# Kernel optimization log

Measured on AMD Instinct MI355X. Metric: run time of the kernel, lower is better.

## Reference

```python
import jax, jax.numpy as jnp
import numpy as np

LL = 1 << 20            # Fastfood padded size (power of 2 >= DD)
DD = 1024 * 768         # out_features * in_features
OUT, IN = 1024, 768


def fwht(v):
    """Unnormalized fast Walsh-Hadamard transform over a length-2^k vector."""
    n = v.shape[0]
    h = 1
    while h < n:
        v = v.reshape(-1, 2, h)
        v = jnp.concatenate([v[:, 0] + v[:, 1], v[:, 0] - v[:, 1]], axis=-1)
        h *= 2
    return v.reshape(n)


def setup_inputs() -> dict:
    key = jax.random.key(0)
    ks = jax.random.split(key, 7)
    x = jax.random.normal(ks[0], (8, 2048, IN), dtype=jnp.float32)
    theta = jax.random.normal(ks[1], (2048,), dtype=jnp.float32)
    W_0 = jax.random.normal(ks[2], (OUT, IN), dtype=jnp.float32) * 0.02
    b = jax.random.normal(ks[3], (OUT,), dtype=jnp.float32) * 0.02
    # Rademacher +/-1 diagonal
    BB = (jax.random.bernoulli(ks[4], 0.5, (LL,)).astype(jnp.float32) * 2.0 - 1.0)
    GG = jax.random.normal(ks[5], (LL,), dtype=jnp.float32)
    Pi = jax.random.permutation(ks[6], LL).astype(jnp.int64)
    return {"x": x, "theta": theta, "W_0": W_0, "b": b, "BB": BB, "GG": GG, "Pi": Pi}


def reference(x, theta, W_0, b, BB, GG, Pi):
    # pad intrinsic parameter to LL (theta.numel() < LL branch)
    theta_pad = jnp.zeros((LL,), dtype=theta.dtype).at[: theta.shape[0]].set(theta)
    # Fastfood: H B theta -> permute -> G diag -> H
    v = fwht(BB * theta_pad)
    v = v[Pi] * GG
    v = fwht(v)
    divisor = jnp.sqrt(LL * jnp.sum(GG * GG))
    update_vec = v[:DD] / (divisor * np.sqrt(float(DD) / LL))
    W_eff = W_0 + update_vec.reshape(OUT, IN)
    return jnp.einsum("bsi,oi->bso", x, W_eff) + b
```

## Files before the change

### kernel.cpp

```cpp
#include <hip/hip_runtime.h>
#include <hip/hip_bf16.h>


#define LL (1 << 20)
#define DD (1024 * 768)
#define OUTF 1024
#define INF 768
#define MROWS 16384

typedef __attribute__((ext_vector_type(8))) short s16x8;
typedef __attribute__((ext_vector_type(4))) float f32x4;
typedef __attribute__((ext_vector_type(16))) float f32x16;

__device__ __forceinline__ unsigned short f2bf(float f) {
    union { float f; unsigned u; } v; v.f = f;
    unsigned r = v.u + 0x7FFF + ((v.u >> 16) & 1);
    return (unsigned short)(r >> 16);
}

__global__ void k3_gather_fwht_lo(const int* __restrict__ Pi, const float* __restrict__ GG,
                                  const float* __restrict__ BB, const float* __restrict__ theta,
                                  const float* __restrict__ X, ushort* __restrict__ XB,
                                  float* __restrict__ T, float* __restrict__ partial) {
    __shared__ float s[1024];
    __shared__ float r01s[2048];
    __shared__ float ws4[4];
    const int tid = threadIdx.x;
    const int row = blockIdx.x;
    const int4   pv = ((const int4*)Pi)[row * 256 + tid];
    const float4 gv = ((const float4*)GG)[row * 256 + tid];
    for (int j = tid; j < 2048; j += 256) r01s[j] = BB[j] * theta[j];
    for (int h = 1; h < 1024; h <<= 1) {
        __syncthreads();
        for (int w = tid; w < 1024; w += 256) {
            int rr = w >> 9;
            int b  = w & 511;
            int bh = b & (h - 1);
            int i  = ((b - bh) << 1) + bh + rr * 1024;
            float a = r01s[i], c = r01s[i + h];
            r01s[i] = a + c; r01s[i + h] = a - c;
        }
    }
    float g2 = gv.x * gv.x + gv.y * gv.y + gv.z * gv.z + gv.w * gv.w;
    #pragma unroll
    for (int o = 32; o > 0; o >>= 1) g2 += __shfl_down(g2, o, 64);
    if ((tid & 63) == 0) ws4[tid >> 6] = g2;
    __syncthreads();
    {
        int p; float g, v;
        p = pv.x; g = gv.x;
        v = (r01s[p & 1023] + (((p >> 10) & 1) ? -1.0f : 1.0f) * r01s[1024 + (p & 1023)]) * g;
        s[tid * 4 + 0] = v;
        p = pv.y; g = gv.y;
        v = (r01s[p & 1023] + (((p >> 10) & 1) ? -1.0f : 1.0f) * r01s[1024 + (p & 1023)]) * g;
        s[tid * 4 + 1] = v;
        p = pv.z; g = gv.z;
        v = (r01s[p & 1023] + (((p >> 10) & 1) ? -1.0f : 1.0f) * r01s[1024 + (p & 1023)]) * g;
        s[tid * 4 + 2] = v;
        p = pv.w; g = gv.w;
        v = (r01s[p & 1023] + (((p >> 10) & 1) ? -1.0f : 1.0f) * r01s[1024 + (p & 1023)]) * g;
        s[tid * 4 + 3] = v;
    }
    for (int h = 1; h < 1024; h <<= 1) {
        __syncthreads();
        for (int w = tid; w < 512; w += 256) {
            int bh = w & (h - 1);
            int i  = ((w - bh) << 1) + bh;
            float a = s[i], c = s[i + h];
            s[i] = a + c; s[i + h] = a - c;
        }
    }
    __syncthreads();
    float4 v;
    v.x = s[tid * 4 + 0]; v.y = s[tid * 4 + 1]; v.z = s[tid * 4 + 2]; v.w = s[tid * 4 + 3];
    ((float4*)T)[row * 256 + tid] = v;
    if (tid == 0) partial[row] = ws4[0] + ws4[1] + ws4[2] + ws4[3];

    const float4* X4 = (const float4*)X + (size_t)row * 3072;
    ushort4* XB4 = (ushort4*)XB + (size_t)row * 3072;
    #pragma unroll
    for (int j = 0; j < 12; j++) {
        float4 xv = X4[j * 256 + tid];
        ushort4 o;
        o.x = f2bf(xv.x); o.y = f2bf(xv.y); o.z = f2bf(xv.z); o.w = f2bf(xv.w);
        XB4[j * 256 + tid] = o;
    }
}

__global__ void k4_fwht_hi(const float* __restrict__ T, const float* __restrict__ partial,
                           const float* __restrict__ W0, ushort* __restrict__ WB) {
    __shared__ float s[8 * 1025];
    __shared__ float rw[5];
    const int tid = threadIdx.x;
    float p = partial[tid] + partial[tid + 256] + partial[tid + 512] + partial[tid + 768];
    #pragma unroll
    for (int o = 32; o > 0; o >>= 1) p += __shfl_down(p, o, 64);
    if ((tid & 63) == 0) rw[tid >> 6] = p;

    const int lo0 = blockIdx.x * 8;
    const float4* T4 = (const float4*)T;
    const int hio = tid >> 1;
    const int q   = tid & 1;
    for (int hb = 0; hb < 8; hb++) {
        int hi = hb * 128 + hio;
        float4 v = T4[hi * 256 + (lo0 >> 2) + q];
        s[(4 * q + 0) * 1025 + hi] = v.x;
        s[(4 * q + 1) * 1025 + hi] = v.y;
        s[(4 * q + 2) * 1025 + hi] = v.z;
        s[(4 * q + 3) * 1025 + hi] = v.w;
    }
    __syncthreads();
    if (tid == 0) rw[4] = rw[0] + rw[1] + rw[2] + rw[3];
    for (int h = 1; h < 1024; h <<= 1) {
        for (int w = tid; w < 8 * 512; w += 256) {
            int col = w >> 9;
            int b   = w & 511;
            int bh  = b & (h - 1);
            int i   = ((b - bh) << 1) + bh;
            float* pp = s + col * 1025;
            float a = pp[i], c = pp[i + h];
            pp[i] = a + c; pp[i + h] = a - c;
        }
        __syncthreads();
    }
    const float scale = rsqrtf(rw[4] * (float)DD);
    for (int hb = 0; hb < 6; hb++) {
        int hi = hb * 128 + hio;
        int d  = hi * 1024 + lo0 + 4 * q;
        float4 w = *(const float4*)&W0[d];
        ushort4 o;
        o.x = f2bf(w.x + s[(4 * q + 0) * 1025 + hi] * scale);
        o.y = f2bf(w.y + s[(4 * q + 1) * 1025 + hi] * scale);
        o.z = f2bf(w.z + s[(4 * q + 2) * 1025 + hi] * scale);
        o.w = f2bf(w.w + s[(4 * q + 3) * 1025 + hi] * scale);
        *(ushort4*)&WB[d] = o;
    }
}

#define BM 128
#define BN 128
#define BK 64

__global__ __launch_bounds__(256)
void k7_gemm(const ushort* __restrict__ A, const ushort* __restrict__ B,
             const float* __restrict__ bias, float* __restrict__ C) {
    __shared__ ushort As[BM * BK];
    __shared__ ushort Bs[BN * BK];
    const int tid  = threadIdx.x;
    const int lane = tid & 63;
    const int wave = tid >> 6;
    const int m0 = blockIdx.x * BM;
    const int n0 = blockIdx.y * BN;
    const int wm = (wave & 1) * 64;
    const int wn = (wave >> 1) * 64;

    const int fr_row = lane & 31;
    const int fr_kh  = lane >> 5;

    f32x16 acc[2][2];
    #pragma unroll
    for (int i = 0; i < 2; i++)
        #pragma unroll
        for (int j = 0; j < 2; j++) acc[i][j] = (f32x16)(0.0f);

    for (int kt = 0; kt < INF; kt += BK) {
        #pragma unroll
        for (int i = 0; i < 4; i++) {
            const int s   = i * 256 + tid;
            const int row = s >> 3;
            const int kc  = (s & 7) ^ (row & 7);
            const ushort* ga = A + (size_t)(m0 + row) * INF + kt + kc * 8;
            const ushort* gb = B + (size_t)(n0 + row) * INF + kt + kc * 8;
            __builtin_amdgcn_global_load_lds(
                (const __attribute__((address_space(1))) void*)ga,
                (__attribute__((address_space(3))) void*)&As[i * 2048 + wave * 512], 16, 0, 0);
            __builtin_amdgcn_global_load_lds(
                (const __attribute__((address_space(1))) void*)gb,
                (__attribute__((address_space(3))) void*)&Bs[i * 2048 + wave * 512], 16, 0, 0);
        }
        __syncthreads();

        #pragma unroll
        for (int ks = 0; ks < 4; ks++) {
            const int kc = ks * 2 + fr_kh;
            s16x8 af[2], bf[2];
            #pragma unroll
            for (int mi = 0; mi < 2; mi++) {
                const int r = wm + mi * 32 + fr_row;
                af[mi] = *(const s16x8*)&As[(r * 8 + (kc ^ (r & 7))) * 8];
            }
            #pragma unroll
            for (int ni = 0; ni < 2; ni++) {
                const int r = wn + ni * 32 + fr_row;
                bf[ni] = *(const s16x8*)&Bs[(r * 8 + (kc ^ (r & 7))) * 8];
            }
            #pragma unroll
            for (int mi = 0; mi < 2; mi++)
                #pragma unroll
                for (int ni = 0; ni < 2; ni++)
                    acc[mi][ni] = __builtin_amdgcn_mfma_f32_32x32x16_bf16(
                        af[mi], bf[ni], acc[mi][ni], 0, 0, 0);
        }
        __syncthreads();
    }

    const int ccol = lane & 31;
    const int rbase = (lane >> 5) * 4;
    #pragma unroll
    for (int ni = 0; ni < 2; ni++) {
        const int n = n0 + wn + ni * 32 + ccol;
        const float bv = bias[n];
        #pragma unroll
        for (int mi = 0; mi < 2; mi++) {
            const int mb = m0 + wm + mi * 32 + rbase;
            #pragma unroll
            for (int r = 0; r < 16; r++) {
                const int m = mb + (r & 3) + 8 * (r >> 2);
                C[(size_t)m * OUTF + n] = acc[mi][ni][r] + bv;
            }
        }
    }
}

extern "C" void kernel_launch(void* const* d_in, const int* in_sizes, int n_in,
                              void* d_out, int out_size, void* d_ws, size_t ws_size,
                              hipStream_t stream) {
    (void)in_sizes; (void)n_in; (void)out_size; (void)ws_size;
    const float* x     = (const float*)d_in[0];
    const float* theta = (const float*)d_in[1];
    const float* W0    = (const float*)d_in[2];
    const float* bias  = (const float*)d_in[3];
    const float* BB    = (const float*)d_in[4];
    const float* GG    = (const float*)d_in[5];
    const int*   Pi    = (const int*)d_in[6];
    float* out = (float*)d_out;

    char* ws = (char*)d_ws;
    ushort* XB   = (ushort*)ws;
    float*  T    = (float*)(ws + 25165824);
    ushort* WB   = (ushort*)(ws + 29360128);
    float*  PART = (float*)(ws + 30932992);

    k3_gather_fwht_lo<<<1024, 256, 0, stream>>>(Pi, GG, BB, theta, x, XB, T, PART);
    k4_fwht_hi<<<128, 256, 0, stream>>>(T, PART, W0, WB);
    k7_gemm  <<<dim3(MROWS/BM, OUTF/BN), 256, 0, stream>>>(XB, WB, bias, out);
}
```

Before: 177.3 us.

## Fuse x fp32-to-bf16 conversion into GEMM A-tile loads

Removes the separate pass that converts x to bf16 in the gather kernel and writes a bf16 copy to workspace. The GEMM now loads fp32 x tiles straight into LDS with a swizzled layout and packs them to bf16 in registers just before the MFMA. This drops a 50MB read plus 25MB write round trip. In exchange, the GEMM reads twice the A bytes per tile, and since each x tile is reused by 8 column blocks the fp32 traffic is multiplied. It also doubles A's LDS footprint and adds conversion ALU work in the inner loop. Rounding changes from round-to-nearest-even to round-half-up.

```diff
diff --git a/kernel.cpp b/kernel.cpp
--- a/kernel.cpp
+++ b/kernel.cpp
@@ -18,9 +18,14 @@
     return (unsigned short)(r >> 16);
 }
 
+__device__ __forceinline__ unsigned pkbf(float lo, float hi) {
+    union { float f; unsigned u; } a, b;
+    a.f = lo; b.f = hi;
+    return ((a.u + 0x8000u) >> 16) | ((b.u + 0x8000u) & 0xFFFF0000u);
+}
+
 __global__ void k3_gather_fwht_lo(const int* __restrict__ Pi, const float* __restrict__ GG,
                                   const float* __restrict__ BB, const float* __restrict__ theta,
-                                  const float* __restrict__ X, ushort* __restrict__ XB,
                                   float* __restrict__ T, float* __restrict__ partial) {
     __shared__ float s[1024];
     __shared__ float r01s[2048];
@@ -75,16 +80,6 @@
     v.x = s[tid * 4 + 0]; v.y = s[tid * 4 + 1]; v.z = s[tid * 4 + 2]; v.w = s[tid * 4 + 3];
     ((float4*)T)[row * 256 + tid] = v;
     if (tid == 0) partial[row] = ws4[0] + ws4[1] + ws4[2] + ws4[3];
-
-    const float4* X4 = (const float4*)X + (size_t)row * 3072;
-    ushort4* XB4 = (ushort4*)XB + (size_t)row * 3072;
-    #pragma unroll
-    for (int j = 0; j < 12; j++) {
-        float4 xv = X4[j * 256 + tid];
-        ushort4 o;
-        o.x = f2bf(xv.x); o.y = f2bf(xv.y); o.z = f2bf(xv.z); o.w = f2bf(xv.w);
-        XB4[j * 256 + tid] = o;
-    }
 }
 
 __global__ void k4_fwht_hi(const float* __restrict__ T, const float* __restrict__ partial,
@@ -142,10 +137,10 @@
 #define BK 64
 
 __global__ __launch_bounds__(256)
-void k7_gemm(const ushort* __restrict__ A, const ushort* __restrict__ B,
+void k7_gemm(const float* __restrict__ A, const ushort* __restrict__ B,
              const float* __restrict__ bias, float* __restrict__ C) {
-    __shared__ ushort As[BM * BK];
-    __shared__ ushort Bs[BN * BK];
+    __shared__ float  AsF[BM * BK];
+    __shared__ ushort Bs [BN * BK];
     const int tid  = threadIdx.x;
     const int lane = tid & 63;
     const int wave = tid >> 6;
@@ -165,15 +160,21 @@
 
     for (int kt = 0; kt < INF; kt += BK) {
         #pragma unroll
+        for (int i = 0; i < 8; i++) {
+            const int s   = i * 256 + tid;
+            const int row = s >> 4;
+            const int c4  = (s & 15) ^ (row & 15);
+            const float* ga = A + (size_t)(m0 + row) * INF + kt + c4 * 4;
+            __builtin_amdgcn_global_load_lds(
+                (const __attribute__((address_space(1))) void*)ga,
+                (__attribute__((address_space(3))) void*)&AsF[(i * 256 + wave * 64) * 4], 16, 0, 0);
+        }
+        #pragma unroll
         for (int i = 0; i < 4; i++) {
             const int s   = i * 256 + tid;
             const int row = s >> 3;
             const int kc  = (s & 7) ^ (row & 7);
-            const ushort* ga = A + (size_t)(m0 + row) * INF + kt + kc * 8;
             const ushort* gb = B + (size_t)(n0 + row) * INF + kt + kc * 8;
-            __builtin_amdgcn_global_load_lds(
-                (const __attribute__((address_space(1))) void*)ga,
-                (__attribute__((address_space(3))) void*)&As[i * 2048 + wave * 512], 16, 0, 0);
             __builtin_amdgcn_global_load_lds(
                 (const __attribute__((address_space(1))) void*)gb,
                 (__attribute__((address_space(3))) void*)&Bs[i * 2048 + wave * 512], 16, 0, 0);
@@ -182,16 +183,24 @@
 
         #pragma unroll
         for (int ks = 0; ks < 4; ks++) {
-            const int kc = ks * 2 + fr_kh;
             s16x8 af[2], bf[2];
             #pragma unroll
             for (int mi = 0; mi < 2; mi++) {
-                const int r = wm + mi * 32 + fr_row;
-                af[mi] = *(const s16x8*)&As[(r * 8 + (kc ^ (r & 7))) * 8];
+                const int r  = wm + mi * 32 + fr_row;
+                const int c0 = ks * 4 + fr_kh * 2;
+                f32x4 a0 = *(const f32x4*)&AsF[(r * 16 + ((c0 + 0) ^ (r & 15))) * 4];
+                f32x4 a1 = *(const f32x4*)&AsF[(r * 16 + ((c0 + 1) ^ (r & 15))) * 4];
+                union { uint4 u; s16x8 v; } cvt;
+                cvt.u.x = pkbf(a0[0], a0[1]);
+                cvt.u.y = pkbf(a0[2], a0[3]);
+                cvt.u.z = pkbf(a1[0], a1[1]);
+                cvt.u.w = pkbf(a1[2], a1[3]);
+                af[mi] = cvt.v;
             }
             #pragma unroll
             for (int ni = 0; ni < 2; ni++) {
-                const int r = wn + ni * 32 + fr_row;
+                const int r  = wn + ni * 32 + fr_row;
+                const int kc = ks * 2 + fr_kh;
                 bf[ni] = *(const s16x8*)&Bs[(r * 8 + (kc ^ (r & 7))) * 8];
             }
             #pragma unroll
@@ -236,12 +245,11 @@
     float* out = (float*)d_out;
 
     char* ws = (char*)d_ws;
-    ushort* XB   = (ushort*)ws;
-    float*  T    = (float*)(ws + 25165824);
-    ushort* WB   = (ushort*)(ws + 29360128);
-    float*  PART = (float*)(ws + 30932992);
-
-    k3_gather_fwht_lo<<<1024, 256, 0, stream>>>(Pi, GG, BB, theta, x, XB, T, PART);
+    float*  T    = (float*)ws;
+    ushort* WB   = (ushort*)(ws + 4194304);
+    float*  PART = (float*)(ws + 5767168);
+
+    k3_gather_fwht_lo<<<1024, 256, 0, stream>>>(Pi, GG, BB, theta, T, PART);
     k4_fwht_hi<<<128, 256, 0, stream>>>(T, PART, W0, WB);
-    k7_gemm  <<<dim3(MROWS/BM, OUTF/BN), 256, 0, stream>>>(XB, WB, bias, out);
-}
+    k7_gemm  <<<dim3(MROWS/BM, OUTF/BN), 256, 0, stream>>>(x, WB, bias, out);
+}
```

Result: slower. 185.6 us (+4.7%).

## Prefetch next K-tile into registers while computing current tile in GEMM

Applied to the files above, without the earlier changes.

Replaces the direct global-to-LDS loads with register-staged loads. The next K tile is fetched from global memory into registers before the MFMA loop runs on the current LDS tile, then written to LDS after a barrier. This hides global load latency behind compute with a single LDS buffer. In exchange it uses more VGPRs, adds a second barrier per iteration, and gives up the async LDS-direct load path.

```diff
diff --git a/kernel.cpp b/kernel.cpp
--- a/kernel.cpp
+++ b/kernel.cpp
@@ -157,29 +157,47 @@
     const int fr_row = lane & 31;
     const int fr_kh  = lane >> 5;
 
+    const ushort* gA[4];
+    const ushort* gB[4];
+    int lds_off[4];
+    #pragma unroll
+    for (int i = 0; i < 4; i++) {
+        const int s   = i * 256 + tid;
+        const int row = s >> 3;
+        const int kc  = (s & 7) ^ (row & 7);
+        gA[i] = A + (size_t)(m0 + row) * INF + kc * 8;
+        gB[i] = B + (size_t)(n0 + row) * INF + kc * 8;
+        lds_off[i] = s * 8;
+    }
+
     f32x16 acc[2][2];
     #pragma unroll
     for (int i = 0; i < 2; i++)
         #pragma unroll
         for (int j = 0; j < 2; j++) acc[i][j] = (f32x16)(0.0f);
 
-    for (int kt = 0; kt < INF; kt += BK) {
-        #pragma unroll
-        for (int i = 0; i < 4; i++) {
-            const int s   = i * 256 + tid;
-            const int row = s >> 3;
-            const int kc  = (s & 7) ^ (row & 7);
-            const ushort* ga = A + (size_t)(m0 + row) * INF + kt + kc * 8;
-            const ushort* gb = B + (size_t)(n0 + row) * INF + kt + kc * 8;
-            __builtin_amdgcn_global_load_lds(
-                (const __attribute__((address_space(1))) void*)ga,
-                (__attribute__((address_space(3))) void*)&As[i * 2048 + wave * 512], 16, 0, 0);
-            __builtin_amdgcn_global_load_lds(
-                (const __attribute__((address_space(1))) void*)gb,
-                (__attribute__((address_space(3))) void*)&Bs[i * 2048 + wave * 512], 16, 0, 0);
-        }
-        __syncthreads();
-
+    uint4 ra[4], rb[4];
+    #pragma unroll
+    for (int i = 0; i < 4; i++) {
+        ra[i] = *(const uint4*)(gA[i]);
+        rb[i] = *(const uint4*)(gB[i]);
+    }
+    #pragma unroll
+    for (int i = 0; i < 4; i++) {
+        *(uint4*)&As[lds_off[i]] = ra[i];
+        *(uint4*)&Bs[lds_off[i]] = rb[i];
+    }
+    __syncthreads();
+
+    for (int kt = BK; kt <= INF; kt += BK) {
+        const bool last = (kt == INF);
+        if (!last) {
+            #pragma unroll
+            for (int i = 0; i < 4; i++) {
+                ra[i] = *(const uint4*)(gA[i] + kt);
+                rb[i] = *(const uint4*)(gB[i] + kt);
+            }
+        }
         #pragma unroll
         for (int ks = 0; ks < 4; ks++) {
             const int kc = ks * 2 + fr_kh;
@@ -201,7 +219,15 @@
                     acc[mi][ni] = __builtin_amdgcn_mfma_f32_32x32x16_bf16(
                         af[mi], bf[ni], acc[mi][ni], 0, 0, 0);
         }
-        __syncthreads();
+        if (!last) {
+            __syncthreads();
+            #pragma unroll
+            for (int i = 0; i < 4; i++) {
+                *(uint4*)&As[lds_off[i]] = ra[i];
+                *(uint4*)&Bs[lds_off[i]] = rb[i];
+            }
+            __syncthreads();
+        }
     }
 
     const int ccol = lane & 31;
```

After: 256.6 us. 44.8% more time.
